# Performance work log

Measured on AMD Instinct MI355X. Metric: run time of the kernel, lower is better.

## Reference

```python
import jax, jax.numpy as jnp
import numpy as np

N_HEADS, D_MODEL, D_HEAD = 16, 1024, 64
INIT_STD = 0.02


def setup_inputs() -> dict:
    key = jax.random.key(0)
    ks = jax.random.split(key, 5)
    x = jax.random.normal(ks[0], (4, 2048, D_MODEL), dtype=jnp.float32)
    W_Q = jax.random.normal(ks[1], (N_HEADS, D_MODEL, D_HEAD), dtype=jnp.float32) * INIT_STD
    W_K = jax.random.normal(ks[2], (N_HEADS, D_MODEL, D_HEAD), dtype=jnp.float32) * INIT_STD
    W_V = jax.random.normal(ks[3], (N_HEADS, D_MODEL, D_HEAD), dtype=jnp.float32) * INIT_STD
    W_O = jax.random.normal(ks[4], (N_HEADS, D_HEAD, D_MODEL), dtype=jnp.float32) * INIT_STD
    b_Q = jnp.zeros((N_HEADS, D_HEAD), dtype=jnp.float32)
    b_K = jnp.zeros((N_HEADS, D_HEAD), dtype=jnp.float32)
    b_V = jnp.zeros((N_HEADS, D_HEAD), dtype=jnp.float32)
    b_O = jnp.zeros((D_MODEL,), dtype=jnp.float32)
    return {"normalized_resid_pre": x, "W_Q": W_Q, "W_K": W_K, "W_V": W_V,
            "W_O": W_O, "b_Q": b_Q, "b_K": b_K, "b_V": b_V, "b_O": b_O}


def reference(normalized_resid_pre, W_Q, W_K, W_V, W_O, b_Q, b_K, b_V, b_O):
    x = normalized_resid_pre  # [b, s, d_model]
    q = jnp.einsum('bsm,hmd->bshd', x, W_Q) + b_Q  # [b, s, h, d_head]
    k = jnp.einsum('bsm,hmd->bshd', x, W_K) + b_K
    v = jnp.einsum('bsm,hmd->bshd', x, W_V) + b_V
    scores = jnp.einsum('bqhd,bkhd->bhqk', q, k) / jnp.sqrt(jnp.float32(D_HEAD))
    S = x.shape[1]
    causal = jnp.tril(jnp.ones((S, S), dtype=bool))  # keep key_pos <= query_pos
    scores = jnp.where(causal, scores, jnp.finfo(scores.dtype).min)
    pattern = jax.nn.softmax(scores, axis=-1)  # [b, h, q, k]
    z = jnp.einsum('bhqk,bkhd->bqhd', pattern, v)
    attn_out = jnp.einsum('bqhd,hdm->bqm', z, W_O) + b_O
    return attn_out
```

## Files before the change

kernel.cpp:

```cpp
#include <hip/hip_runtime.h>
#include <hip/hip_bf16.h>
#include <math.h>

typedef __bf16 bf16_t;
typedef bf16_t bf16x8 __attribute__((ext_vector_type(8)));
typedef float f32x4 __attribute__((ext_vector_type(4)));

#define BB 4
#define SS 2048
#define HH 16
#define DMODEL 1024
#define DHEAD 64

#define QSCALE 0.18033688011112042f

__device__ inline unsigned short f2bf(float f) {
    union { __hip_bfloat16 h; unsigned short u; } cvt;
    cvt.h = __float2bfloat16(f);
    return cvt.u;
}

__device__ __forceinline__ void gll16(const unsigned short* g, unsigned short* l) {
    __builtin_amdgcn_global_load_lds(
        (const __attribute__((address_space(1))) unsigned int*)(g),
        (__attribute__((address_space(3))) unsigned int*)(l), 16, 0, 0);
}


__global__ void pack_x(const float* __restrict__ x, unsigned short* __restrict__ xb) {
    int i = blockIdx.x * 256 + threadIdx.x;
    const float4 v = ((const float4*)x)[i];
    unsigned short o[4] = { f2bf(v.x), f2bf(v.y), f2bf(v.z), f2bf(v.w) };
    *(uint2*)(xb + 4 * (size_t)i) = *(uint2*)o;
}

__global__ void pack_wqkv(const float* __restrict__ wq, const float* __restrict__ wk,
                          const float* __restrict__ wv, unsigned short* __restrict__ out) {
    int idx = blockIdx.x * 256 + threadIdx.x;
    int k  = idx & 1023;
    int n  = idx >> 10;
    int mat = n >> 10;
    int n1 = n & 1023;
    int h = n1 >> 6, d = n1 & 63;
    const float* w = (mat == 0) ? wq : (mat == 1) ? wk : wv;
    out[idx] = f2bf(w[(h << 16) + (k << 6) + d]);
}

__global__ void pack_wo(const float* __restrict__ wo, unsigned short* __restrict__ out) {
    int idx = blockIdx.x * 256 + threadIdx.x;
    int k = idx & 1023, n = idx >> 10;
    out[idx] = f2bf(wo[(k << 10) + n]);
}


template <bool SWAP>
__device__ __forceinline__ void mf16(f32x4& d, bf16x8 a, bf16x8 b) {
    if constexpr (SWAP)
        d = __builtin_amdgcn_mfma_f32_16x16x32_bf16(b, a, d, 0, 0, 0);
    else
        d = __builtin_amdgcn_mfma_f32_16x16x32_bf16(a, b, d, 0, 0, 0);
}

#define GBAR()   __builtin_amdgcn_s_barrier()
#define SCHEDB() __builtin_amdgcn_sched_barrier(0)
#define WLGKM0() asm volatile("s_waitcnt lgkmcnt(0)" ::: "memory")

template <bool SWAP>
__device__ __forceinline__ void kloop256(
    unsigned short (*sAb)[256][64], unsigned short (*sBb)[256][64],
    const unsigned short* gA0, const unsigned short* gA1,
    const unsigned short* gB0, const unsigned short* gB1,
    int w, int wr, int wc, int l15, int quad, int lo,
    f32x4 (&acc)[8][4])
{
    auto STAGE = [&](const unsigned short* g, unsigned short* lb, int T) {
        const unsigned short* s = g + T * 64;
        gll16(s, lb + w * 8 * 64);
        gll16(s + 64 * 1024, lb + (64 + w * 8) * 64);
    };

    STAGE(gB0, &sBb[0][0][0],   0);
    STAGE(gA0, &sAb[0][0][0],   0);
    STAGE(gB1, &sBb[0][128][0], 0);
    STAGE(gA1, &sAb[0][128][0], 0);
    STAGE(gB0, &sBb[1][0][0],   1);
    STAGE(gA0, &sAb[1][0][0],   1);
    asm volatile("s_waitcnt vmcnt(4)" ::: "memory");
    GBAR();

#pragma unroll 2
    for (int kt = 0; kt < 16; ++kt) {
        const int bsel = kt & 1;
        unsigned short (*A)[64] = sAb[bsel];
        unsigned short (*B)[64] = sBb[bsel];
        bf16x8 a0[4][2], a1[4][2], bA[2][2], bB[2][2];

#pragma unroll
        for (int mi = 0; mi < 4; mi++) {
            a0[mi][0] = *(const bf16x8*)&A[wr * 128 + mi * 16 + l15][(quad ^ lo) * 8];
            a0[mi][1] = *(const bf16x8*)&A[wr * 128 + mi * 16 + l15][((4 | quad) ^ lo) * 8];
        }
#pragma unroll
        for (int nj = 0; nj < 2; nj++) {
            bA[nj][0] = *(const bf16x8*)&B[wc * 64 + nj * 16 + l15][(quad ^ lo) * 8];
            bA[nj][1] = *(const bf16x8*)&B[wc * 64 + nj * 16 + l15][((4 | quad) ^ lo) * 8];
        }
        if (kt + 1 < 16) STAGE(gB1, &sBb[(kt + 1) & 1][128][0], kt + 1);
        GBAR();
        WLGKM0();
        SCHEDB();
        __builtin_amdgcn_s_setprio(1);
#pragma unroll
        for (int mi = 0; mi < 4; mi++)
#pragma unroll
            for (int nj = 0; nj < 2; nj++) {
                mf16<SWAP>(acc[mi][nj], a0[mi][0], bA[nj][0]);
                mf16<SWAP>(acc[mi][nj], a0[mi][1], bA[nj][1]);
            }
        __builtin_amdgcn_s_setprio(0);
        SCHEDB();
        GBAR();

#pragma unroll
        for (int nj = 0; nj < 2; nj++) {
            bB[nj][0] = *(const bf16x8*)&B[wc * 64 + (nj + 2) * 16 + l15][(quad ^ lo) * 8];
            bB[nj][1] = *(const bf16x8*)&B[wc * 64 + (nj + 2) * 16 + l15][((4 | quad) ^ lo) * 8];
        }
        if (kt + 1 < 16) STAGE(gA1, &sAb[(kt + 1) & 1][128][0], kt + 1);
        GBAR();
        WLGKM0();
        SCHEDB();
        __builtin_amdgcn_s_setprio(1);
#pragma unroll
        for (int mi = 0; mi < 4; mi++)
#pragma unroll
            for (int nj = 0; nj < 2; nj++) {
                mf16<SWAP>(acc[mi][nj + 2], a0[mi][0], bB[nj][0]);
                mf16<SWAP>(acc[mi][nj + 2], a0[mi][1], bB[nj][1]);
            }
        __builtin_amdgcn_s_setprio(0);
        SCHEDB();
        GBAR();

#pragma unroll
        for (int mi = 0; mi < 4; mi++) {
            a1[mi][0] = *(const bf16x8*)&A[wr * 128 + 64 + mi * 16 + l15][(quad ^ lo) * 8];
            a1[mi][1] = *(const bf16x8*)&A[wr * 128 + 64 + mi * 16 + l15][((4 | quad) ^ lo) * 8];
        }
        if (kt + 2 < 16) STAGE(gB0, &sBb[kt & 1][0][0], kt + 2);
        GBAR();
        WLGKM0();
        SCHEDB();
        __builtin_amdgcn_s_setprio(1);
#pragma unroll
        for (int mi = 0; mi < 4; mi++)
#pragma unroll
            for (int nj = 0; nj < 2; nj++) {
                mf16<SWAP>(acc[4 + mi][nj + 2], a1[mi][0], bB[nj][0]);
                mf16<SWAP>(acc[4 + mi][nj + 2], a1[mi][1], bB[nj][1]);
            }
        __builtin_amdgcn_s_setprio(0);
        SCHEDB();
        GBAR();

        if (kt + 2 < 16) STAGE(gA0, &sAb[kt & 1][0][0], kt + 2);
        GBAR();
        WLGKM0();
        SCHEDB();
        __builtin_amdgcn_s_setprio(1);
#pragma unroll
        for (int mi = 0; mi < 4; mi++)
#pragma unroll
            for (int nj = 0; nj < 2; nj++) {
                mf16<SWAP>(acc[4 + mi][nj], a1[mi][0], bA[nj][0]);
                mf16<SWAP>(acc[4 + mi][nj], a1[mi][1], bA[nj][1]);
            }
        __builtin_amdgcn_s_setprio(0);
        SCHEDB();
        if (kt == 14) {
            asm volatile("s_waitcnt vmcnt(0)" ::: "memory");
        } else if (kt < 14) {
            asm volatile("s_waitcnt vmcnt(4)" ::: "memory");
        }
        GBAR();
    }
}

__global__ __launch_bounds__(512, 2) void gemm_qkv8(
    const unsigned short* __restrict__ xb,
    const unsigned short* __restrict__ wT,
    const float* __restrict__ bq, const float* __restrict__ bk, const float* __restrict__ bv,
    unsigned short* __restrict__ qws, unsigned short* __restrict__ kws,
    unsigned short* __restrict__ vtw)
{
    __shared__ __align__(16) unsigned short sA[2][256][64];
    __shared__ __align__(16) unsigned short sB[2][256][64];

    const int t = threadIdx.x;
    const int lane = t & 63;
    const int w = t >> 6;
    const int quad = lane >> 4;
    const int l15 = lane & 15;
    const int lo = l15 & 7;
    const int wr = w >> 2;
    const int wc = w & 3;
    const int n0 = blockIdx.x * 256;
    const int m0 = blockIdx.y * 256;
    const int mat = n0 >> 10;

    const int sr8 = lane >> 3;
    const size_t soff = (size_t)(w * 8 + sr8) * 1024 + (size_t)(((lane & 7) ^ sr8) * 8);
    const unsigned short* gA0 = xb + (size_t)m0 * 1024 + soff;
    const unsigned short* gA1 = xb + (size_t)(m0 + 128) * 1024 + soff;
    const unsigned short* gB0 = wT + (size_t)n0 * 1024 + soff;
    const unsigned short* gB1 = wT + (size_t)(n0 + 128) * 1024 + soff;

    f32x4 acc[8][4] = {};

    const int b = m0 >> 11;
    const int m0r = m0 & 2047;

    if (mat != 2) {
        kloop256<true>(sA, sB, gA0, gA1, gB0, gB1, w, wr, wc, l15, quad, lo, acc);
        const float* bias_p = (mat == 0) ? bq : bk;
        const float scale = (mat == 0) ? QSCALE : 1.0f;
        unsigned short* dst = (mat == 0) ? qws : kws;
#pragma unroll
        for (int nj = 0; nj < 4; nj++) {
            const int noff = wc * 64 + nj * 16 + quad * 4;
            const int nmat = (n0 & 1023) + noff;
            const int h = nmat >> 6;
            const int dbase = nmat & 63;
            const float4 bv4 = *(const float4*)(bias_p + h * 64 + dbase);
            const float bias_r[4] = { bv4.x, bv4.y, bv4.z, bv4.w };
#pragma unroll
            for (int mig = 0; mig < 8; mig++) {
                const int s = m0r + wr * 128 + mig * 16 + l15;
                unsigned short pk[4];
#pragma unroll
                for (int r = 0; r < 4; r++) pk[r] = f2bf((acc[mig][nj][r] + bias_r[r]) * scale);
                *(uint2*)(dst + (size_t)((b * 16 + h) * 2048 + s) * 64 + dbase) = *(uint2*)pk;
            }
        }
    } else {
        kloop256<false>(sA, sB, gA0, gA1, gB0, gB1, w, wr, wc, l15, quad, lo, acc);
#pragma unroll
        for (int nj = 0; nj < 4; nj++) {
            const int n1 = (n0 & 1023) + wc * 64 + nj * 16 + l15;
            const int h = n1 >> 6, d = n1 & 63;
            const float bias = bv[h * 64 + d];
#pragma unroll
            for (int mig = 0; mig < 8; mig++) {
                const int s0 = m0r + wr * 128 + mig * 16 + quad * 4;
                unsigned short pk[4];
#pragma unroll
                for (int r = 0; r < 4; r++) pk[r] = f2bf(acc[mig][nj][r] + bias);
                *(uint2*)(vtw + ((size_t)(b * 16 + h) * 64 + d) * 2048 + s0) = *(uint2*)pk;
            }
        }
    }
}


__global__ __launch_bounds__(256) void attn3(
    const unsigned short* __restrict__ qws,
    const unsigned short* __restrict__ kws,
    const unsigned short* __restrict__ vtw,
    unsigned short* __restrict__ zb)
{
    __shared__ __align__(16) unsigned short Ks[64 * 64];
    __shared__ __align__(16) unsigned short Vs[64 * 64];
    __shared__ __align__(16) unsigned short Ps[4 * 16 * 64];

    const int t = threadIdx.x;
    const int lane = t & 63;
    const int w = t >> 6;
    const int quad = lane >> 4;
    const int l15 = lane & 15;
    const int hi = l15 >> 3;
    const int lo = l15 & 7;

    const int qt = 31 - (blockIdx.x >> 6);
    const int bh = blockIdx.x & 63;
    const int q0 = qt * 64;
    const int qbase = q0 + w * 16;
    const size_t base = (size_t)bh * SS * DHEAD;
    const unsigned short* Q = qws + base;
    const unsigned short* K = kws + base;
    const unsigned short* Vt = vtw + base;

    bf16x8 qf0 = *(const bf16x8*)(Q + (size_t)(qbase + l15) * 64 + quad * 8);
    bf16x8 qf1 = *(const bf16x8*)(Q + (size_t)(qbase + l15) * 64 + 32 + quad * 8);

    f32x4 o[4] = {};
    float lsum[4] = {0.f, 0.f, 0.f, 0.f};
    unsigned short* Pw = Ps + w * 16 * 64;

    const int sr = t >> 2;
    const int g0 = t & 3;
    const int sw0 = ((g0 ^ (sr & 7)) << 3);
    const int sw1 = (((g0 + 4) ^ (sr & 7)) << 3);
    unsigned short* ksw = Ks + sr * 64;
    unsigned short* vsw = Vs + sr * 64;
    const unsigned short* Kg = K + (size_t)sr * 64 + g0 * 8;
    const unsigned short* Vg = Vt + (size_t)sr * 2048 + g0 * 8;

    const int gq0 = ((quad ^ lo) << 3);
    const int gq1 = (((quad + 4) ^ lo) << 3);

    const int nch = qt + 1;

    uint4 kr0 = *(const uint4*)(Kg);
    uint4 kr1 = *(const uint4*)(Kg + 32);
    uint4 vr0 = *(const uint4*)(Vg);
    uint4 vr1 = *(const uint4*)(Vg + 32);

    for (int c = 0; c < nch; c++) {
        __builtin_amdgcn_sched_barrier(0);
        __builtin_amdgcn_s_barrier();
        *(uint4*)(ksw + sw0) = kr0;
        *(uint4*)(ksw + sw1) = kr1;
        *(uint4*)(vsw + sw0) = vr0;
        *(uint4*)(vsw + sw1) = vr1;
        if (c + 1 < nch) {
            const unsigned short* kp = Kg + (size_t)(c + 1) * 64 * 64;
            const unsigned short* vp = Vg + (size_t)(c + 1) * 64;
            kr0 = *(const uint4*)(kp);
            kr1 = *(const uint4*)(kp + 32);
            vr0 = *(const uint4*)(vp);
            vr1 = *(const uint4*)(vp + 32);
        }
        asm volatile("s_waitcnt lgkmcnt(0)" ::: "memory");
        __builtin_amdgcn_s_barrier();
        __builtin_amdgcn_sched_barrier(0);

        f32x4 s[4];
        __builtin_amdgcn_s_setprio(1);
#pragma unroll
        for (int sub = 0; sub < 4; sub++) {
            const unsigned short* kr = Ks + (sub * 16 + l15) * 64;
            bf16x8 kf0 = *(const bf16x8*)(kr + gq0);
            bf16x8 kf1 = *(const bf16x8*)(kr + gq1);
            f32x4 sv = {};
            sv = __builtin_amdgcn_mfma_f32_16x16x32_bf16(qf0, kf0, sv, 0, 0, 0);
            sv = __builtin_amdgcn_mfma_f32_16x16x32_bf16(qf1, kf1, sv, 0, 0, 0);
            s[sub] = sv;
        }
        __builtin_amdgcn_s_setprio(0);

        const int kb = c * 64;
        if (c == nch - 1) {
            const int qg = qbase + quad * 4;
#pragma unroll
            for (int sub = 0; sub < 4; sub++) {
                const int key = kb + sub * 16 + l15;
#pragma unroll
                for (int r = 0; r < 4; r++) {
                    float p = (key > qg + r) ? 0.f : exp2f(s[sub][r]);
                    lsum[r] += p;
                    const int q = quad * 4 + r;
                    Pw[q * 64 + (((sub * 2 + hi) ^ (q & 7)) << 3) + lo] = f2bf(p);
                }
            }
        } else {
#pragma unroll
            for (int sub = 0; sub < 4; sub++)
#pragma unroll
                for (int r = 0; r < 4; r++) {
                    float p = exp2f(s[sub][r]);
                    lsum[r] += p;
                    const int q = quad * 4 + r;
                    Pw[q * 64 + (((sub * 2 + hi) ^ (q & 7)) << 3) + lo] = f2bf(p);
                }
        }
        asm volatile("s_waitcnt lgkmcnt(0)" ::: "memory");
        bf16x8 pf0 = *(const bf16x8*)(Pw + l15 * 64 + gq0);
        bf16x8 pf1 = *(const bf16x8*)(Pw + l15 * 64 + gq1);
        __builtin_amdgcn_s_setprio(1);
#pragma unroll
        for (int dt = 0; dt < 4; dt++) {
            const unsigned short* vrp = Vs + (dt * 16 + l15) * 64;
            bf16x8 vf0 = *(const bf16x8*)(vrp + gq0);
            bf16x8 vf1 = *(const bf16x8*)(vrp + gq1);
            o[dt] = __builtin_amdgcn_mfma_f32_16x16x32_bf16(vf0, pf0, o[dt], 0, 0, 0);
            o[dt] = __builtin_amdgcn_mfma_f32_16x16x32_bf16(vf1, pf1, o[dt], 0, 0, 0);
        }
        __builtin_amdgcn_s_setprio(0);
    }

#pragma unroll
    for (int r = 0; r < 4; r++) {
        float v = lsum[r];
        v += __shfl_xor(v, 1);
        v += __shfl_xor(v, 2);
        v += __shfl_xor(v, 4);
        v += __shfl_xor(v, 8);
        lsum[r] = v;
    }
    const int srcl = (l15 >> 2) << 4;
    float t0 = __shfl(lsum[0], srcl);
    float t1 = __shfl(lsum[1], srcl);
    float t2 = __shfl(lsum[2], srcl);
    float t3 = __shfl(lsum[3], srcl);
    const int rr = l15 & 3;
    float den = (rr == 0) ? t0 : (rr == 1) ? t1 : (rr == 2) ? t2 : t3;
    const float inv = 1.0f / den;

    const int b = bh >> 4, h = bh & 15;
    const int q = qbase + l15;
    unsigned short* zrow = zb + (size_t)(b * 2048 + q) * 1024 + h * 64 + quad * 4;
#pragma unroll
    for (int dt = 0; dt < 4; dt++) {
        unsigned short pk[4];
#pragma unroll
        for (int r = 0; r < 4; r++) pk[r] = f2bf(o[dt][r] * inv);
        *(uint2*)(zrow + dt * 16) = *(uint2*)pk;
    }
}


__global__ __launch_bounds__(256) void gemm_out(
    const unsigned short* __restrict__ zb,
    const unsigned short* __restrict__ wT,
    const float* __restrict__ bo,
    float* __restrict__ out)
{
    __shared__ __align__(16) unsigned short lA[128 * 32];
    __shared__ __align__(16) unsigned short lB[128 * 32];
    const int t = threadIdx.x;
    const int lane = t & 63;
    const int w = t >> 6;
    const int quad = lane >> 4;
    const int l15 = lane & 15;
    const int n0 = blockIdx.x * 128;
    const int m0 = blockIdx.y * 128;
    const int wm = (w >> 1) * 64;
    const int wn = (w & 1) * 64;

    f32x4 acc[4][4] = {};

    const int srow = w * 16 + (lane >> 2);
    const int scol = (lane & 3) * 8;
    const unsigned short* Ag0 = zb + (size_t)(m0 + srow) * 1024 + scol;
    const unsigned short* Ag1 = Ag0 + (size_t)64 * 1024;
    const unsigned short* Bg0 = wT + (size_t)(n0 + srow) * 1024 + scol;
    const unsigned short* Bg1 = Bg0 + (size_t)64 * 1024;
    unsigned short* lA0 = lA + (w * 16) * 32;
    unsigned short* lA1 = lA + (64 + w * 16) * 32;
    unsigned short* lB0 = lB + (w * 16) * 32;
    unsigned short* lB1 = lB + (64 + w * 16) * 32;

    for (int kt = 0; kt < 1024; kt += 32) {
        __syncthreads();
        gll16(Ag0 + kt, lA0);
        gll16(Ag1 + kt, lA1);
        gll16(Bg0 + kt, lB0);
        gll16(Bg1 + kt, lB1);
        __syncthreads();
        bf16x8 af[4], bfr[4];
#pragma unroll
        for (int i = 0; i < 4; i++) {
            af[i]  = *(const bf16x8*)(lA + (wm + i * 16 + l15) * 32 + quad * 8);
            bfr[i] = *(const bf16x8*)(lB + (wn + i * 16 + l15) * 32 + quad * 8);
        }
#pragma unroll
        for (int i = 0; i < 4; i++)
#pragma unroll
            for (int j = 0; j < 4; j++)
                acc[i][j] = __builtin_amdgcn_mfma_f32_16x16x32_bf16(bfr[j], af[i], acc[i][j], 0, 0, 0);
    }

#pragma unroll
    for (int j = 0; j < 4; j++) {
        const int nbase = n0 + wn + j * 16 + quad * 4;
        const float4 bv4 = *(const float4*)(bo + nbase);
#pragma unroll
        for (int i = 0; i < 4; i++) {
            const int s = m0 + wm + i * 16 + l15;
            float4 v;
            v.x = acc[i][j][0] + bv4.x;
            v.y = acc[i][j][1] + bv4.y;
            v.z = acc[i][j][2] + bv4.z;
            v.w = acc[i][j][3] + bv4.w;
            *(float4*)(out + (size_t)s * 1024 + nbase) = v;
        }
    }
}


extern "C" void kernel_launch(void* const* d_in, const int* in_sizes, int n_in,
                              void* d_out, int out_size, void* d_ws, size_t ws_size,
                              hipStream_t stream) {
    const float* x  = (const float*)d_in[0];
    const float* WQ = (const float*)d_in[1];
    const float* WK = (const float*)d_in[2];
    const float* WV = (const float*)d_in[3];
    const float* WO = (const float*)d_in[4];
    const float* bQ = (const float*)d_in[5];
    const float* bK = (const float*)d_in[6];
    const float* bV = (const float*)d_in[7];
    const float* bO = (const float*)d_in[8];
    float* out = (float*)d_out;

    char* ws = (char*)d_ws;
    unsigned short* xb   = (unsigned short*)ws;
    unsigned short* wqkv = (unsigned short*)(ws + (16u << 20));
    unsigned short* woT  = (unsigned short*)(ws + (22u << 20));
    unsigned short* qws  = (unsigned short*)(ws + (24u << 20));
    unsigned short* kws  = (unsigned short*)(ws + (40u << 20));
    unsigned short* vtw  = (unsigned short*)(ws + (56u << 20));
    unsigned short* zbuf = xb;

    pack_x<<<8192, 256, 0, stream>>>(x, xb);
    pack_wqkv<<<(3072 * 1024) / 256, 256, 0, stream>>>(WQ, WK, WV, wqkv);
    pack_wo<<<(1024 * 1024) / 256, 256, 0, stream>>>(WO, woT);
    gemm_qkv8<<<dim3(12, 32), 512, 0, stream>>>(xb, wqkv, bQ, bK, bV, qws, kws, vtw);
    attn3<<<2048, 256, 0, stream>>>(qws, kws, vtw, zbuf);
    gemm_out<<<dim3(8, 64), 256, 0, stream>>>(zbuf, woT, bO, out);
}
```

Measured before the change: 306.2 us.

## Replace output projection GEMM with 256x256 pipelined 8-wave kernel

The simple 128x128 single-buffered output projection GEMM is replaced by a new gemm_out8 that reuses the double-buffered, phase-interleaved 256x256 k-loop already used for the QKV projection. The k-loop is also refactored into explicit ping-pong ktstep calls with separate LDS buffers instead of a bsel-indexed loop. The aim is more data reuse per tile and overlap of global loads with MFMA work in the output GEMM. The trade-off is only 128 blocks for 256 CUs, so fewer CUs stay busy, and higher register and LDS use per block.

```diff
diff --git a/kernel.cpp b/kernel.cpp
--- a/kernel.cpp
+++ b/kernel.cpp
@@ -65,126 +65,140 @@
 #define SCHEDB() __builtin_amdgcn_sched_barrier(0)
 #define WLGKM0() asm volatile("s_waitcnt lgkmcnt(0)" ::: "memory")
 
+__device__ __forceinline__ void stage2(const unsigned short* g, unsigned short* lb,
+                                       int T, int w) {
+    const unsigned short* s = g + T * 64;
+    gll16(s, lb + w * 8 * 64);
+    gll16(s + 64 * 1024, lb + (64 + w * 8) * 64);
+}
+
+template <bool SWAP>
+__device__ __forceinline__ void ktstep(
+    unsigned short (*Ac)[64], unsigned short (*Bc)[64],
+    unsigned short (*An)[64], unsigned short (*Bn)[64],
+    const unsigned short* gA0, const unsigned short* gA1,
+    const unsigned short* gB0, const unsigned short* gB1,
+    int kt, int w, int wr, int wc, int l15, int quad, int lo,
+    f32x4 (&acc)[8][4])
+{
+    bf16x8 a0f[4][2], a1f[4][2], bAf[2][2], bBf[2][2];
+    const int c0 = (quad ^ lo) * 8;
+    const int c1 = ((4 | quad) ^ lo) * 8;
+
+#pragma unroll
+    for (int mi = 0; mi < 4; mi++) {
+        a0f[mi][0] = *(const bf16x8*)&Ac[wr * 128 + mi * 16 + l15][c0];
+        a0f[mi][1] = *(const bf16x8*)&Ac[wr * 128 + mi * 16 + l15][c1];
+    }
+#pragma unroll
+    for (int nj = 0; nj < 2; nj++) {
+        bAf[nj][0] = *(const bf16x8*)&Bc[wc * 64 + nj * 16 + l15][c0];
+        bAf[nj][1] = *(const bf16x8*)&Bc[wc * 64 + nj * 16 + l15][c1];
+    }
+    if (kt + 1 < 16) stage2(gB1, &Bn[128][0], kt + 1, w);
+    GBAR();
+    WLGKM0();
+    SCHEDB();
+    __builtin_amdgcn_s_setprio(1);
+#pragma unroll
+    for (int mi = 0; mi < 4; mi++)
+#pragma unroll
+        for (int nj = 0; nj < 2; nj++) {
+            mf16<SWAP>(acc[mi][nj], a0f[mi][0], bAf[nj][0]);
+            mf16<SWAP>(acc[mi][nj], a0f[mi][1], bAf[nj][1]);
+        }
+    __builtin_amdgcn_s_setprio(0);
+    SCHEDB();
+    GBAR();
+
+#pragma unroll
+    for (int nj = 0; nj < 2; nj++) {
+        bBf[nj][0] = *(const bf16x8*)&Bc[wc * 64 + (nj + 2) * 16 + l15][c0];
+        bBf[nj][1] = *(const bf16x8*)&Bc[wc * 64 + (nj + 2) * 16 + l15][c1];
+    }
+    if (kt + 1 < 16) stage2(gA1, &An[128][0], kt + 1, w);
+    GBAR();
+    WLGKM0();
+    SCHEDB();
+    __builtin_amdgcn_s_setprio(1);
+#pragma unroll
+    for (int mi = 0; mi < 4; mi++)
+#pragma unroll
+        for (int nj = 0; nj < 2; nj++) {
+            mf16<SWAP>(acc[mi][nj + 2], a0f[mi][0], bBf[nj][0]);
+            mf16<SWAP>(acc[mi][nj + 2], a0f[mi][1], bBf[nj][1]);
+        }
+    __builtin_amdgcn_s_setprio(0);
+    SCHEDB();
+    GBAR();
+
+#pragma unroll
+    for (int mi = 0; mi < 4; mi++) {
+        a1f[mi][0] = *(const bf16x8*)&Ac[wr * 128 + 64 + mi * 16 + l15][c0];
+        a1f[mi][1] = *(const bf16x8*)&Ac[wr * 128 + 64 + mi * 16 + l15][c1];
+    }
+    if (kt + 2 < 16) stage2(gB0, &Bc[0][0], kt + 2, w);
+    GBAR();
+    WLGKM0();
+    SCHEDB();
+    __builtin_amdgcn_s_setprio(1);
+#pragma unroll
+    for (int mi = 0; mi < 4; mi++)
+#pragma unroll
+        for (int nj = 0; nj < 2; nj++) {
+            mf16<SWAP>(acc[4 + mi][nj + 2], a1f[mi][0], bBf[nj][0]);
+            mf16<SWAP>(acc[4 + mi][nj + 2], a1f[mi][1], bBf[nj][1]);
+        }
+    __builtin_amdgcn_s_setprio(0);
+    SCHEDB();
+    GBAR();
+
+    if (kt + 2 < 16) stage2(gA0, &Ac[0][0], kt + 2, w);
+    GBAR();
+    WLGKM0();
+    SCHEDB();
+    __builtin_amdgcn_s_setprio(1);
+#pragma unroll
+    for (int mi = 0; mi < 4; mi++)
+#pragma unroll
+        for (int nj = 0; nj < 2; nj++) {
+            mf16<SWAP>(acc[4 + mi][nj], a1f[mi][0], bAf[nj][0]);
+            mf16<SWAP>(acc[4 + mi][nj], a1f[mi][1], bAf[nj][1]);
+        }
+    __builtin_amdgcn_s_setprio(0);
+    SCHEDB();
+    if (kt == 14) {
+        asm volatile("s_waitcnt vmcnt(0)" ::: "memory");
+    } else if (kt < 14) {
+        asm volatile("s_waitcnt vmcnt(4)" ::: "memory");
+    }
+    GBAR();
+}
+
 template <bool SWAP>
 __device__ __forceinline__ void kloop256(
-    unsigned short (*sAb)[256][64], unsigned short (*sBb)[256][64],
+    unsigned short (*A0)[64], unsigned short (*A1)[64],
+    unsigned short (*B0)[64], unsigned short (*B1)[64],
     const unsigned short* gA0, const unsigned short* gA1,
     const unsigned short* gB0, const unsigned short* gB1,
     int w, int wr, int wc, int l15, int quad, int lo,
     f32x4 (&acc)[8][4])
 {
-    auto STAGE = [&](const unsigned short* g, unsigned short* lb, int T) {
-        const unsigned short* s = g + T * 64;
-        gll16(s, lb + w * 8 * 64);
-        gll16(s + 64 * 1024, lb + (64 + w * 8) * 64);
-    };
-
-    STAGE(gB0, &sBb[0][0][0],   0);
-    STAGE(gA0, &sAb[0][0][0],   0);
-    STAGE(gB1, &sBb[0][128][0], 0);
-    STAGE(gA1, &sAb[0][128][0], 0);
-    STAGE(gB0, &sBb[1][0][0],   1);
-    STAGE(gA0, &sAb[1][0][0],   1);
+    stage2(gB0, &B0[0][0],   0, w);
+    stage2(gA0, &A0[0][0],   0, w);
+    stage2(gB1, &B0[128][0], 0, w);
+    stage2(gA1, &A0[128][0], 0, w);
+    stage2(gB0, &B1[0][0],   1, w);
+    stage2(gA0, &A1[0][0],   1, w);
     asm volatile("s_waitcnt vmcnt(4)" ::: "memory");
     GBAR();
 
-#pragma unroll 2
-    for (int kt = 0; kt < 16; ++kt) {
-        const int bsel = kt & 1;
-        unsigned short (*A)[64] = sAb[bsel];
-        unsigned short (*B)[64] = sBb[bsel];
-        bf16x8 a0[4][2], a1[4][2], bA[2][2], bB[2][2];
-
-#pragma unroll
-        for (int mi = 0; mi < 4; mi++) {
-            a0[mi][0] = *(const bf16x8*)&A[wr * 128 + mi * 16 + l15][(quad ^ lo) * 8];
-            a0[mi][1] = *(const bf16x8*)&A[wr * 128 + mi * 16 + l15][((4 | quad) ^ lo) * 8];
-        }
-#pragma unroll
-        for (int nj = 0; nj < 2; nj++) {
-            bA[nj][0] = *(const bf16x8*)&B[wc * 64 + nj * 16 + l15][(quad ^ lo) * 8];
-            bA[nj][1] = *(const bf16x8*)&B[wc * 64 + nj * 16 + l15][((4 | quad) ^ lo) * 8];
-        }
-        if (kt + 1 < 16) STAGE(gB1, &sBb[(kt + 1) & 1][128][0], kt + 1);
-        GBAR();
-        WLGKM0();
-        SCHEDB();
-        __builtin_amdgcn_s_setprio(1);
-#pragma unroll
-        for (int mi = 0; mi < 4; mi++)
-#pragma unroll
-            for (int nj = 0; nj < 2; nj++) {
-                mf16<SWAP>(acc[mi][nj], a0[mi][0], bA[nj][0]);
-                mf16<SWAP>(acc[mi][nj], a0[mi][1], bA[nj][1]);
-            }
-        __builtin_amdgcn_s_setprio(0);
-        SCHEDB();
-        GBAR();
-
-#pragma unroll
-        for (int nj = 0; nj < 2; nj++) {
-            bB[nj][0] = *(const bf16x8*)&B[wc * 64 + (nj + 2) * 16 + l15][(quad ^ lo) * 8];
-            bB[nj][1] = *(const bf16x8*)&B[wc * 64 + (nj + 2) * 16 + l15][((4 | quad) ^ lo) * 8];
-        }
-        if (kt + 1 < 16) STAGE(gA1, &sAb[(kt + 1) & 1][128][0], kt + 1);
-        GBAR();
-        WLGKM0();
-        SCHEDB();
-        __builtin_amdgcn_s_setprio(1);
-#pragma unroll
-        for (int mi = 0; mi < 4; mi++)
-#pragma unroll
-            for (int nj = 0; nj < 2; nj++) {
-                mf16<SWAP>(acc[mi][nj + 2], a0[mi][0], bB[nj][0]);
-                mf16<SWAP>(acc[mi][nj + 2], a0[mi][1], bB[nj][1]);
-            }
-        __builtin_amdgcn_s_setprio(0);
-        SCHEDB();
-        GBAR();
-
-#pragma unroll
-        for (int mi = 0; mi < 4; mi++) {
-            a1[mi][0] = *(const bf16x8*)&A[wr * 128 + 64 + mi * 16 + l15][(quad ^ lo) * 8];
-            a1[mi][1] = *(const bf16x8*)&A[wr * 128 + 64 + mi * 16 + l15][((4 | quad) ^ lo) * 8];
-        }
-        if (kt + 2 < 16) STAGE(gB0, &sBb[kt & 1][0][0], kt + 2);
-        GBAR();
-        WLGKM0();
-        SCHEDB();
-        __builtin_amdgcn_s_setprio(1);
-#pragma unroll
-        for (int mi = 0; mi < 4; mi++)
-#pragma unroll
-            for (int nj = 0; nj < 2; nj++) {
-                mf16<SWAP>(acc[4 + mi][nj + 2], a1[mi][0], bB[nj][0]);
-                mf16<SWAP>(acc[4 + mi][nj + 2], a1[mi][1], bB[nj][1]);
-            }
-        __builtin_amdgcn_s_setprio(0);
-        SCHEDB();
-        GBAR();
-
-        if (kt + 2 < 16) STAGE(gA0, &sAb[kt & 1][0][0], kt + 2);
-        GBAR();
-        WLGKM0();
-        SCHEDB();
-        __builtin_amdgcn_s_setprio(1);
-#pragma unroll
-        for (int mi = 0; mi < 4; mi++)
-#pragma unroll
-            for (int nj = 0; nj < 2; nj++) {
-                mf16<SWAP>(acc[4 + mi][nj], a1[mi][0], bA[nj][0]);
-                mf16<SWAP>(acc[4 + mi][nj], a1[mi][1], bA[nj][1]);
-            }
-        __builtin_amdgcn_s_setprio(0);
-        SCHEDB();
-        if (kt == 14) {
-            asm volatile("s_waitcnt vmcnt(0)" ::: "memory");
-        } else if (kt < 14) {
-            asm volatile("s_waitcnt vmcnt(4)" ::: "memory");
-        }
-        GBAR();
-    }
-}
+    for (int i = 0; i < 8; ++i) {
+        ktstep<SWAP>(A0, B0, A1, B1, gA0, gA1, gB0, gB1, 2 * i,     w, wr, wc, l15, quad, lo, acc);
+        ktstep<SWAP>(A1, B1, A0, B0, gA0, gA1, gB0, gB1, 2 * i + 1, w, wr, wc, l15, quad, lo, acc);
+    }
+}
+
 
 __global__ __launch_bounds__(512, 2) void gemm_qkv8(
     const unsigned short* __restrict__ xb,
@@ -193,8 +207,10 @@
     unsigned short* __restrict__ qws, unsigned short* __restrict__ kws,
     unsigned short* __restrict__ vtw)
 {
-    __shared__ __align__(16) unsigned short sA[2][256][64];
-    __shared__ __align__(16) unsigned short sB[2][256][64];
+    __shared__ __align__(16) unsigned short A0s[256][64];
+    __shared__ __align__(16) unsigned short A1s[256][64];
+    __shared__ __align__(16) unsigned short B0s[256][64];
+    __shared__ __align__(16) unsigned short B1s[256][64];
 
     const int t = threadIdx.x;
     const int lane = t & 63;
@@ -221,7 +237,7 @@
     const int m0r = m0 & 2047;
 
     if (mat != 2) {
-        kloop256<true>(sA, sB, gA0, gA1, gB0, gB1, w, wr, wc, l15, quad, lo, acc);
+        kloop256<true>(A0s, A1s, B0s, B1s, gA0, gA1, gB0, gB1, w, wr, wc, l15, quad, lo, acc);
         const float* bias_p = (mat == 0) ? bq : bk;
         const float scale = (mat == 0) ? QSCALE : 1.0f;
         unsigned short* dst = (mat == 0) ? qws : kws;
@@ -243,7 +259,7 @@
             }
         }
     } else {
-        kloop256<false>(sA, sB, gA0, gA1, gB0, gB1, w, wr, wc, l15, quad, lo, acc);
+        kloop256<false>(A0s, A1s, B0s, B1s, gA0, gA1, gB0, gB1, w, wr, wc, l15, quad, lo, acc);
 #pragma unroll
         for (int nj = 0; nj < 4; nj++) {
             const int n1 = (n0 & 1023) + wc * 64 + nj * 16 + l15;
@@ -257,6 +273,57 @@
                 for (int r = 0; r < 4; r++) pk[r] = f2bf(acc[mig][nj][r] + bias);
                 *(uint2*)(vtw + ((size_t)(b * 16 + h) * 64 + d) * 2048 + s0) = *(uint2*)pk;
             }
+        }
+    }
+}
+
+
+__global__ __launch_bounds__(512, 2) void gemm_out8(
+    const unsigned short* __restrict__ zb,
+    const unsigned short* __restrict__ wT,
+    const float* __restrict__ bo,
+    float* __restrict__ out)
+{
+    __shared__ __align__(16) unsigned short A0s[256][64];
+    __shared__ __align__(16) unsigned short A1s[256][64];
+    __shared__ __align__(16) unsigned short B0s[256][64];
+    __shared__ __align__(16) unsigned short B1s[256][64];
+
+    const int t = threadIdx.x;
+    const int lane = t & 63;
+    const int w = t >> 6;
+    const int quad = lane >> 4;
+    const int l15 = lane & 15;
+    const int lo = l15 & 7;
+    const int wr = w >> 2;
+    const int wc = w & 3;
+    const int n0 = blockIdx.x * 256;
+    const int m0 = blockIdx.y * 256;
+
+    const int sr8 = lane >> 3;
+    const size_t soff = (size_t)(w * 8 + sr8) * 1024 + (size_t)(((lane & 7) ^ sr8) * 8);
+    const unsigned short* gA0 = zb + (size_t)m0 * 1024 + soff;
+    const unsigned short* gA1 = zb + (size_t)(m0 + 128) * 1024 + soff;
+    const unsigned short* gB0 = wT + (size_t)n0 * 1024 + soff;
+    const unsigned short* gB1 = wT + (size_t)(n0 + 128) * 1024 + soff;
+
+    f32x4 acc[8][4] = {};
+
+    kloop256<true>(A0s, A1s, B0s, B1s, gA0, gA1, gB0, gB1, w, wr, wc, l15, quad, lo, acc);
+
+#pragma unroll
+    for (int nj = 0; nj < 4; nj++) {
+        const int nbase = n0 + wc * 64 + nj * 16 + quad * 4;
+        const float4 bv4 = *(const float4*)(bo + nbase);
+#pragma unroll
+        for (int mig = 0; mig < 8; mig++) {
+            const int s = m0 + wr * 128 + mig * 16 + l15;
+            float4 v;
+            v.x = acc[mig][nj][0] + bv4.x;
+            v.y = acc[mig][nj][1] + bv4.y;
+            v.z = acc[mig][nj][2] + bv4.z;
+            v.w = acc[mig][nj][3] + bv4.w;
+            *(float4*)(out + (size_t)s * 1024 + nbase) = v;
         }
     }
 }
@@ -419,75 +486,6 @@
 }
 
 
-__global__ __launch_bounds__(256) void gemm_out(
-    const unsigned short* __restrict__ zb,
-    const unsigned short* __restrict__ wT,
-    const float* __restrict__ bo,
-    float* __restrict__ out)
-{
-    __shared__ __align__(16) unsigned short lA[128 * 32];
-    __shared__ __align__(16) unsigned short lB[128 * 32];
-    const int t = threadIdx.x;
-    const int lane = t & 63;
-    const int w = t >> 6;
-    const int quad = lane >> 4;
-    const int l15 = lane & 15;
-    const int n0 = blockIdx.x * 128;
-    const int m0 = blockIdx.y * 128;
-    const int wm = (w >> 1) * 64;
-    const int wn = (w & 1) * 64;
-
-    f32x4 acc[4][4] = {};
-
-    const int srow = w * 16 + (lane >> 2);
-    const int scol = (lane & 3) * 8;
-    const unsigned short* Ag0 = zb + (size_t)(m0 + srow) * 1024 + scol;
-    const unsigned short* Ag1 = Ag0 + (size_t)64 * 1024;
-    const unsigned short* Bg0 = wT + (size_t)(n0 + srow) * 1024 + scol;
-    const unsigned short* Bg1 = Bg0 + (size_t)64 * 1024;
-    unsigned short* lA0 = lA + (w * 16) * 32;
-    unsigned short* lA1 = lA + (64 + w * 16) * 32;
-    unsigned short* lB0 = lB + (w * 16) * 32;
-    unsigned short* lB1 = lB + (64 + w * 16) * 32;
-
-    for (int kt = 0; kt < 1024; kt += 32) {
-        __syncthreads();
-        gll16(Ag0 + kt, lA0);
-        gll16(Ag1 + kt, lA1);
-        gll16(Bg0 + kt, lB0);
-        gll16(Bg1 + kt, lB1);
-        __syncthreads();
-        bf16x8 af[4], bfr[4];
-#pragma unroll
-        for (int i = 0; i < 4; i++) {
-            af[i]  = *(const bf16x8*)(lA + (wm + i * 16 + l15) * 32 + quad * 8);
-            bfr[i] = *(const bf16x8*)(lB + (wn + i * 16 + l15) * 32 + quad * 8);
-        }
-#pragma unroll
-        for (int i = 0; i < 4; i++)
-#pragma unroll
-            for (int j = 0; j < 4; j++)
-                acc[i][j] = __builtin_amdgcn_mfma_f32_16x16x32_bf16(bfr[j], af[i], acc[i][j], 0, 0, 0);
-    }
-
-#pragma unroll
-    for (int j = 0; j < 4; j++) {
-        const int nbase = n0 + wn + j * 16 + quad * 4;
-        const float4 bv4 = *(const float4*)(bo + nbase);
-#pragma unroll
-        for (int i = 0; i < 4; i++) {
-            const int s = m0 + wm + i * 16 + l15;
-            float4 v;
-            v.x = acc[i][j][0] + bv4.x;
-            v.y = acc[i][j][1] + bv4.y;
-            v.z = acc[i][j][2] + bv4.z;
-            v.w = acc[i][j][3] + bv4.w;
-            *(float4*)(out + (size_t)s * 1024 + nbase) = v;
-        }
-    }
-}
-
-
 extern "C" void kernel_launch(void* const* d_in, const int* in_sizes, int n_in,
                               void* d_out, int out_size, void* d_ws, size_t ws_size,
                               hipStream_t stream) {
@@ -516,5 +514,5 @@
     pack_wo<<<(1024 * 1024) / 256, 256, 0, stream>>>(WO, woT);
     gemm_qkv8<<<dim3(12, 32), 512, 0, stream>>>(xb, wqkv, bQ, bK, bV, qws, kws, vtw);
     attn3<<<2048, 256, 0, stream>>>(qws, kws, vtw, zbuf);
-    gemm_out<<<dim3(8, 64), 256, 0, stream>>>(zbuf, woT, bO, out);
-}
+    gemm_out8<<<dim3(4, 32), 512, 0, stream>>>(zbuf, woT, bO, out);
+}
```

New measurement: 305.8 us. About the same (-0.1%).
